# Kernel optimization log

Measured on AMD Instinct MI355X. Metric: run time of the kernel, lower is better.

The kernel has to match this reference:

```python
import jax, jax.numpy as jnp
import numpy as np

N = 100000   # nodes
E = 1600000  # edges (avg degree 16)
D = 64       # node_dim == edge_dim == graph_width == emb_dim
L = 3        # num_layer


def setup_inputs() -> dict:
    key = jax.random.key(0)
    ks = jax.random.split(key, 7)
    x = jax.random.normal(ks[0], (N, D), dtype=jnp.float32)
    edge_index = jax.random.randint(ks[1], (2, E), 0, N, dtype=jnp.int32)
    edge_attr = jax.random.normal(ks[2], (E, D), dtype=jnp.float32)
    # per-layer MLP params: Linear(2D -> 2D), ReLU, Linear(2D -> D)
    s1 = 1.0 / np.sqrt(2 * D)
    W1 = jax.random.normal(ks[3], (L, 2 * D, 2 * D), dtype=jnp.float32) * s1
    b1 = jnp.zeros((L, 2 * D), dtype=jnp.float32)
    W2 = jax.random.normal(ks[4], (L, 2 * D, D), dtype=jnp.float32) * s1
    b2 = jnp.zeros((L, D), dtype=jnp.float32)
    return {"x": x, "edge_index": edge_index, "edge_attr": edge_attr,
            "W1": W1, "b1": b1, "W2": W2, "b2": b2}


def reference(x, edge_index, edge_attr, W1, b1, W2, b2):
    n = x.shape[0]
    loop = jnp.arange(n, dtype=edge_index.dtype)
    src = jnp.concatenate([edge_index[0], loop])   # x_j = x[src]
    dst = jnp.concatenate([edge_index[1], loop])   # aggregate at dst
    # self-loop edge attr: zeros with last column = 1
    sl_attr = jnp.zeros((n, edge_attr.shape[1]), x.dtype).at[:, -1].set(1.0)
    ea = jnp.concatenate([edge_attr, sl_attr], axis=0)  # [E+N, D]

    h = x
    for l in range(L):
        msg = jnp.concatenate([ea, h[src]], axis=1)              # [E+N, 2D]
        aggr = jax.ops.segment_sum(msg, dst, num_segments=n)     # [N, 2D]
        hid = jnp.maximum(aggr @ W1[l] + b1[l], 0.0)             # [N, 2D]
        h_new = hid @ W2[l] + b2[l]                              # [N, D]
        if l < L - 1:                                            # ReLU between layers (JK='last')
            h_new = jnp.maximum(h_new, 0.0)
        h = h_new
    return h
```

## Files before the change

### kernel.cpp

```cpp
#include <hip/hip_runtime.h>

typedef unsigned int uint;
typedef unsigned short ushort;

#define WS_ALIGN(x) (((x) + (size_t)255) & ~(size_t)255)

typedef __attribute__((ext_vector_type(8))) short short8;
typedef __attribute__((ext_vector_type(4))) float f32x4;

__device__ __forceinline__ ushort f2bf(float f) {
    uint u = __builtin_bit_cast(uint, f);
    u = (u + 0x7fffu + ((u >> 16) & 1u)) >> 16;
    return (ushort)u;
}
__device__ __forceinline__ uint packbf(float a, float b) {
    return (uint)f2bf(a) | ((uint)f2bf(b) << 16);
}
__device__ __forceinline__ float bflo(uint u) { return __builtin_bit_cast(float, u << 16); }
__device__ __forceinline__ float bfhi(uint u) { return __builtin_bit_cast(float, u & 0xffff0000u); }

__global__ __launch_bounds__(256) void k_prep(const float4* __restrict__ x, ushort4* __restrict__ xh, int n4,
                                              const float* __restrict__ W1, ushort* __restrict__ W1t, int t1,
                                              const float* __restrict__ W2, ushort* __restrict__ W2t, int t2,
                                              int* __restrict__ cnt, int N) {
    int i = blockIdx.x * 256 + threadIdx.x;
    if (i < n4) {
        float4 v = x[i];
        ushort4 o;
        o.x = f2bf(v.x); o.y = f2bf(v.y); o.z = f2bf(v.z); o.w = f2bf(v.w);
        xh[i] = o;
        return;
    }
    int j = i - n4;
    if (j < t1) {
        int kk = j & 127;
        int rem = j >> 7;
        int nn = rem % 128;
        int l = rem / 128;
        W1t[j] = f2bf(W1[((size_t)(l * 128 + kk)) * 128 + nn]);
        return;
    }
    int k2 = j - t1;
    if (k2 < t2) {
        int kk = k2 & 127;
        int rem = k2 >> 7;
        int nn = rem % 64;
        int l = rem / 64;
        W2t[k2] = f2bf(W2[((size_t)(l * 128 + kk)) * 64 + nn]);
        return;
    }
    int z = k2 - t2;
    if (z < N) cnt[z] = 0;
}

__global__ __launch_bounds__(256) void k_fill(const int* __restrict__ ei, int* __restrict__ cnt,
                                              int2* __restrict__ csr, int E) {
    int i = blockIdx.x * 256 + threadIdx.x;
    int e0 = i * 2;
    if (e0 >= E) return;
    int2 ss = *(const int2*)(ei + e0);
    int2 dd = *(const int2*)(ei + E + e0);
    {
        int p = atomicAdd(&cnt[dd.x], 1);
        if (p < 64) csr[((size_t)dd.x << 6) + p] = make_int2(ss.x, e0);
    }
    if (e0 + 1 < E) {
        int p = atomicAdd(&cnt[dd.y], 1);
        if (p < 64) csr[((size_t)dd.y << 6) + p] = make_int2(ss.y, e0 + 1);
    }
}

__device__ __forceinline__ void aggr_edge_body(int wid, int lane, const float* __restrict__ ea,
                                               const int* __restrict__ cnt, const int2* __restrict__ csr,
                                               ushort* __restrict__ aggr_e) {
    const f32x4* ea4 = (const f32x4*)ea;
    const int q = lane >> 4, t = lane & 15;
    int m = cnt[wid]; m = m > 64 ? 64 : m;
    int idx = (lane < m) ? csr[((size_t)wid << 6) + lane].y : 0;
    f32x4 s = (f32x4)(0.f);
    if (q == 0 && t == 15) s[3] = 1.0f;
    int j = 0;
    for (; j + 16 <= m; j += 16) {
        int e0 = __shfl(idx, j + q),     e1 = __shfl(idx, j + 4 + q);
        int e2 = __shfl(idx, j + 8 + q), e3 = __shfl(idx, j + 12 + q);
        f32x4 v0 = __builtin_nontemporal_load(&ea4[(size_t)e0 * 16 + t]);
        f32x4 v1 = __builtin_nontemporal_load(&ea4[(size_t)e1 * 16 + t]);
        f32x4 v2 = __builtin_nontemporal_load(&ea4[(size_t)e2 * 16 + t]);
        f32x4 v3 = __builtin_nontemporal_load(&ea4[(size_t)e3 * 16 + t]);
        s += (v0 + v1) + (v2 + v3);
    }
    for (; j + 4 <= m; j += 4) {
        int e0 = __shfl(idx, j + q);
        s += __builtin_nontemporal_load(&ea4[(size_t)e0 * 16 + t]);
    }
    if (j < m) {
        int e0 = __shfl(idx, j + q);
        if (j + q < m) s += __builtin_nontemporal_load(&ea4[(size_t)e0 * 16 + t]);
    }
    s[0] += __shfl_xor(s[0], 16); s[1] += __shfl_xor(s[1], 16);
    s[2] += __shfl_xor(s[2], 16); s[3] += __shfl_xor(s[3], 16);
    s[0] += __shfl_xor(s[0], 32); s[1] += __shfl_xor(s[1], 32);
    s[2] += __shfl_xor(s[2], 32); s[3] += __shfl_xor(s[3], 32);
    if (q == 0) {
        uint2 o;
        o.x = packbf(s[0], s[1]);
        o.y = packbf(s[2], s[3]);
        *(uint2*)(aggr_e + (size_t)wid * 64 + t * 4) = o;
    }
}

__device__ __forceinline__ void aggr_h_body(int wid, int lane, const ushort* __restrict__ h,
                                            const int* __restrict__ cnt, const int2* __restrict__ csr,
                                            ushort* __restrict__ aggr_h) {
    const uint2* h2 = (const uint2*)h;
    const int q = lane >> 4, t = lane & 15;
    int m = cnt[wid]; m = m > 64 ? 64 : m;
    int idx = (lane < m) ? csr[((size_t)wid << 6) + lane].x : 0;
    float s0 = 0.f, s1 = 0.f, s2 = 0.f, s3 = 0.f;
    if (q == 0) {
        uint2 u = h2[(size_t)wid * 16 + t];
        s0 = bflo(u.x); s1 = bfhi(u.x); s2 = bflo(u.y); s3 = bfhi(u.y);
    }
    int j = 0;
    for (; j + 16 <= m; j += 16) {
        int r0 = __shfl(idx, j + q),     r1 = __shfl(idx, j + 4 + q);
        int r2 = __shfl(idx, j + 8 + q), r3 = __shfl(idx, j + 12 + q);
        uint2 u0 = h2[(size_t)r0 * 16 + t];
        uint2 u1 = h2[(size_t)r1 * 16 + t];
        uint2 u2 = h2[(size_t)r2 * 16 + t];
        uint2 u3 = h2[(size_t)r3 * 16 + t];
        s0 += (bflo(u0.x) + bflo(u1.x)) + (bflo(u2.x) + bflo(u3.x));
        s1 += (bfhi(u0.x) + bfhi(u1.x)) + (bfhi(u2.x) + bfhi(u3.x));
        s2 += (bflo(u0.y) + bflo(u1.y)) + (bflo(u2.y) + bflo(u3.y));
        s3 += (bfhi(u0.y) + bfhi(u1.y)) + (bfhi(u2.y) + bfhi(u3.y));
    }
    for (; j + 4 <= m; j += 4) {
        int r0 = __shfl(idx, j + q);
        uint2 u = h2[(size_t)r0 * 16 + t];
        s0 += bflo(u.x); s1 += bfhi(u.x); s2 += bflo(u.y); s3 += bfhi(u.y);
    }
    if (j < m) {
        int r0 = __shfl(idx, j + q);
        if (j + q < m) {
            uint2 u = h2[(size_t)r0 * 16 + t];
            s0 += bflo(u.x); s1 += bfhi(u.x); s2 += bflo(u.y); s3 += bfhi(u.y);
        }
    }
    s0 += __shfl_xor(s0, 16); s1 += __shfl_xor(s1, 16);
    s2 += __shfl_xor(s2, 16); s3 += __shfl_xor(s3, 16);
    s0 += __shfl_xor(s0, 32); s1 += __shfl_xor(s1, 32);
    s2 += __shfl_xor(s2, 32); s3 += __shfl_xor(s3, 32);
    if (q == 0) {
        uint2 o;
        o.x = packbf(s0, s1);
        o.y = packbf(s2, s3);
        *(uint2*)(aggr_h + (size_t)wid * 64 + t * 4) = o;
    }
}

__global__ __launch_bounds__(256) void k_aggr_combo(const float* __restrict__ ea, const ushort* __restrict__ xh,
                                                    const int* __restrict__ cnt, const int2* __restrict__ csr,
                                                    ushort* __restrict__ aggr_e, ushort* __restrict__ aggr_h,
                                                    int n, int gN4) {
    int lane = threadIdx.x & 63;
    if ((int)blockIdx.x < gN4) {
        int wid = (blockIdx.x * 256 + threadIdx.x) >> 6;
        if (wid < n) aggr_edge_body(wid, lane, ea, cnt, csr, aggr_e);
    } else {
        int wid = ((blockIdx.x - gN4) * 256 + threadIdx.x) >> 6;
        if (wid < n) aggr_h_body(wid, lane, xh, cnt, csr, aggr_h);
    }
}

__global__ __launch_bounds__(256) void k_aggr_h(const ushort* __restrict__ h, const int* __restrict__ cnt,
                                                const int2* __restrict__ csr, ushort* __restrict__ aggr_h, int n) {
    int wid = (blockIdx.x * 256 + threadIdx.x) >> 6;
    int lane = threadIdx.x & 63;
    if (wid >= n) return;
    aggr_h_body(wid, lane, h, cnt, csr, aggr_h);
}

__global__ __launch_bounds__(256) void k_mlp(const ushort* __restrict__ aggr_e,
                                             const ushort* __restrict__ aggr_h,
                                             const ushort* __restrict__ W1t,
                                             const float* __restrict__ b1,
                                             const ushort* __restrict__ W2t,
                                             const float* __restrict__ b2,
                                             float* __restrict__ outf,
                                             ushort* __restrict__ outh,
                                             int n) {
    __shared__ ushort a_s[64][136];
    const int tid = threadIdx.x;
    const int lane = tid & 63;
    const int wv = tid >> 6;
    const int row0 = blockIdx.x * 64;
    const int mrow0 = wv * 16;

    {
        int cc = (lane & 7) * 8;
        int rr = lane >> 3;
#pragma unroll
        for (int p = 0; p < 2; ++p) {
            int r = mrow0 + p * 8 + rr;
            int node = row0 + r;
            short8 ve = (short8)(0), vh = (short8)(0);
            if (node < n) {
                ve = *(const short8*)(aggr_e + (size_t)node * 64 + cc);
                vh = *(const short8*)(aggr_h + (size_t)node * 64 + cc);
            }
            *(short8*)(&a_s[r][cc]) = ve;
            *(short8*)(&a_s[r][64 + cc]) = vh;
        }
    }

    const int arow = mrow0 + (lane & 15);
    const int koff = (lane >> 4) * 8;
    const int drow = mrow0 + (lane >> 4) * 4;

    f32x4 acc[8];
#pragma unroll
    for (int nt = 0; nt < 8; ++nt) acc[nt] = (f32x4)(0.f);
    for (int ks = 0; ks < 4; ++ks) {
        short8 af = *(const short8*)(&a_s[arow][ks * 32 + koff]);
#pragma unroll
        for (int nt = 0; nt < 8; ++nt) {
            short8 bf = *(const short8*)(W1t + (size_t)(nt * 16 + (lane & 15)) * 128 + ks * 32 + koff);
            acc[nt] = __builtin_amdgcn_mfma_f32_16x16x32_bf16(af, bf, acc[nt], 0, 0, 0);
        }
    }
#pragma unroll
    for (int nt = 0; nt < 8; ++nt) {
        int col = nt * 16 + (lane & 15);
        float bias = b1[col];
#pragma unroll
        for (int r = 0; r < 4; ++r) {
            float v = acc[nt][r] + bias;
            v = v > 0.f ? v : 0.f;
            a_s[drow + r][col] = f2bf(v);
        }
    }

    f32x4 acc2[4];
#pragma unroll
    for (int nt = 0; nt < 4; ++nt) acc2[nt] = (f32x4)(0.f);
    for (int ks = 0; ks < 4; ++ks) {
        short8 af = *(const short8*)(&a_s[arow][ks * 32 + koff]);
#pragma unroll
        for (int nt = 0; nt < 4; ++nt) {
            short8 bf = *(const short8*)(W2t + (size_t)(nt * 16 + (lane & 15)) * 128 + ks * 32 + koff);
            acc2[nt] = __builtin_amdgcn_mfma_f32_16x16x32_bf16(af, bf, acc2[nt], 0, 0, 0);
        }
    }
#pragma unroll
    for (int nt = 0; nt < 4; ++nt) {
        int col = nt * 16 + (lane & 15);
        float bias = b2[col];
#pragma unroll
        for (int r = 0; r < 4; ++r) {
            int grow = row0 + drow + r;
            if (grow < n) {
                float v = acc2[nt][r] + bias;
                if (outh) {
                    v = v > 0.f ? v : 0.f;
                    outh[(size_t)grow * 64 + col] = f2bf(v);
                } else {
                    outf[(size_t)grow * 64 + col] = v;
                }
            }
        }
    }
}

extern "C" void kernel_launch(void* const* d_in, const int* in_sizes, int n_in,
                              void* d_out, int out_size, void* d_ws, size_t ws_size,
                              hipStream_t stream) {
    const float* x  = (const float*)d_in[0];
    const int*   ei = (const int*)d_in[1];
    const float* ea = (const float*)d_in[2];
    const float* W1 = (const float*)d_in[3];
    const float* b1 = (const float*)d_in[4];
    const float* W2 = (const float*)d_in[5];
    const float* b2 = (const float*)d_in[6];
    const int N = in_sizes[0] / 64;
    const int E = in_sizes[1] / 2;
    const int L = in_sizes[3] / (128 * 128);

    char* ws = (char*)d_ws;
    size_t o = 0;
    auto carve = [&](size_t bytes) { char* p = ws + o; o += WS_ALIGN(bytes); return p; };
    int*    cnt     = (int*)carve((size_t)N * 4);
    int2*   csr     = (int2*)carve((size_t)N * 64 * 8);
    ushort* aggr_e  = (ushort*)carve((size_t)N * 64 * 2);
    ushort* aggr_h  = (ushort*)carve((size_t)N * 64 * 2);
    ushort* xh      = (ushort*)carve((size_t)N * 64 * 2);
    ushort* hA      = (ushort*)carve((size_t)N * 64 * 2);
    ushort* hB      = (ushort*)carve((size_t)N * 64 * 2);
    ushort* W1t     = (ushort*)carve((size_t)L * 128 * 128 * 2);
    ushort* W2t     = (ushort*)carve((size_t)L * 64 * 128 * 2);

    int n4 = N * 16;
    int t1 = L * 128 * 128;
    int t2 = L * 64 * 128;
    int prep_total = n4 + t1 + t2 + N;
    k_prep<<<(prep_total + 255) / 256, 256, 0, stream>>>((const float4*)x, (ushort4*)xh, n4,
                                                         W1, W1t, t1, W2, W2t, t2, cnt, N);

    int gF = ((E + 1) / 2 + 255) / 256;
    k_fill<<<gF, 256, 0, stream>>>(ei, cnt, csr, E);

    int gN4 = (N + 3) / 4;
    k_aggr_combo<<<2 * gN4, 256, 0, stream>>>(ea, xh, cnt, csr, aggr_e, aggr_h, N, gN4);

    int gM = (N + 63) / 64;
    for (int l = 0; l < L; ++l) {
        if (l > 0) {
            const ushort* hin = (l == 1) ? hA : hB;
            k_aggr_h<<<gN4, 256, 0, stream>>>(hin, cnt, csr, aggr_h, N);
        }
        float*  outf = (l == L - 1) ? (float*)d_out : nullptr;
        ushort* outh = (l == L - 1) ? nullptr : ((l == 0) ? hA : hB);
        k_mlp<<<gM, 256, 0, stream>>>(aggr_e, aggr_h,
                                      W1t + (size_t)l * 128 * 128, b1 + (size_t)l * 128,
                                      W2t + (size_t)l * 64 * 128, b2 + (size_t)l * 64,
                                      outf, outh, N);
    }
}
```

Measured before the change: 473.4 us.

## Fuse neighbor-h aggregation into the MLP kernel for layers after the first

For layers 1 and 2, the separate k_aggr_h pass is replaced by one 1024-thread kernel. Each wave gathers and sums neighbor h rows for four nodes straight into shared memory, then runs both MFMA GEMMs on the 64-row tile, with the hidden activations also held in shared memory. This removes the aggr_h round trip through global memory and one launch per layer. In exchange, each block runs the latency-bound gather serially across only 16 waves, and the larger blocks may lower occupancy or the gather's memory-level parallelism.

```diff
diff --git a/kernel.cpp b/kernel.cpp
--- a/kernel.cpp
+++ b/kernel.cpp
@@ -109,16 +109,15 @@
     }
 }
 
-__device__ __forceinline__ void aggr_h_body(int wid, int lane, const ushort* __restrict__ h,
-                                            const int* __restrict__ cnt, const int2* __restrict__ csr,
-                                            ushort* __restrict__ aggr_h) {
+__device__ __forceinline__ uint2 aggr_h_vals(int node, int lane, const ushort* __restrict__ h,
+                                             const int* __restrict__ cnt, const int2* __restrict__ csr) {
     const uint2* h2 = (const uint2*)h;
     const int q = lane >> 4, t = lane & 15;
-    int m = cnt[wid]; m = m > 64 ? 64 : m;
-    int idx = (lane < m) ? csr[((size_t)wid << 6) + lane].x : 0;
+    int m = cnt[node]; m = m > 64 ? 64 : m;
+    int idx = (lane < m) ? csr[((size_t)node << 6) + lane].x : 0;
     float s0 = 0.f, s1 = 0.f, s2 = 0.f, s3 = 0.f;
     if (q == 0) {
-        uint2 u = h2[(size_t)wid * 16 + t];
+        uint2 u = h2[(size_t)node * 16 + t];
         s0 = bflo(u.x); s1 = bfhi(u.x); s2 = bflo(u.y); s3 = bfhi(u.y);
     }
     int j = 0;
@@ -150,12 +149,17 @@
     s2 += __shfl_xor(s2, 16); s3 += __shfl_xor(s3, 16);
     s0 += __shfl_xor(s0, 32); s1 += __shfl_xor(s1, 32);
     s2 += __shfl_xor(s2, 32); s3 += __shfl_xor(s3, 32);
-    if (q == 0) {
-        uint2 o;
-        o.x = packbf(s0, s1);
-        o.y = packbf(s2, s3);
-        *(uint2*)(aggr_h + (size_t)wid * 64 + t * 4) = o;
-    }
+    uint2 o;
+    o.x = packbf(s0, s1);
+    o.y = packbf(s2, s3);
+    return o;
+}
+
+__device__ __forceinline__ void aggr_h_body(int wid, int lane, const ushort* __restrict__ h,
+                                            const int* __restrict__ cnt, const int2* __restrict__ csr,
+                                            ushort* __restrict__ aggr_h) {
+    uint2 o = aggr_h_vals(wid, lane, h, cnt, csr);
+    if ((lane >> 4) == 0) *(uint2*)(aggr_h + (size_t)wid * 64 + (lane & 15) * 4) = o;
 }
 
 __global__ __launch_bounds__(256) void k_aggr_combo(const float* __restrict__ ea, const ushort* __restrict__ xh,
@@ -172,23 +176,10 @@
     }
 }
 
-__global__ __launch_bounds__(256) void k_aggr_h(const ushort* __restrict__ h, const int* __restrict__ cnt,
-                                                const int2* __restrict__ csr, ushort* __restrict__ aggr_h, int n) {
-    int wid = (blockIdx.x * 256 + threadIdx.x) >> 6;
-    int lane = threadIdx.x & 63;
-    if (wid >= n) return;
-    aggr_h_body(wid, lane, h, cnt, csr, aggr_h);
-}
-
-__global__ __launch_bounds__(256) void k_mlp(const ushort* __restrict__ aggr_e,
-                                             const ushort* __restrict__ aggr_h,
-                                             const ushort* __restrict__ W1t,
-                                             const float* __restrict__ b1,
-                                             const ushort* __restrict__ W2t,
-                                             const float* __restrict__ b2,
-                                             float* __restrict__ outf,
-                                             ushort* __restrict__ outh,
-                                             int n) {
+__global__ __launch_bounds__(256) void k_mlp(const ushort* __restrict__ aggr_e, const ushort* __restrict__ aggr_h,
+                                             const ushort* __restrict__ W1t, const float* __restrict__ b1,
+                                             const ushort* __restrict__ W2t, const float* __restrict__ b2,
+                                             float* __restrict__ outf, ushort* __restrict__ outh, int n) {
     __shared__ ushort a_s[64][136];
     const int tid = threadIdx.x;
     const int lane = tid & 63;
@@ -260,6 +251,93 @@
             int grow = row0 + drow + r;
             if (grow < n) {
                 float v = acc2[nt][r] + bias;
+                if (outh) {
+                    v = v > 0.f ? v : 0.f;
+                    outh[(size_t)grow * 64 + col] = f2bf(v);
+                } else {
+                    outf[(size_t)grow * 64 + col] = v;
+                }
+            }
+        }
+    }
+}
+
+__global__ __launch_bounds__(1024) void k_layer_fused(const ushort* __restrict__ h,
+                                                      const ushort* __restrict__ aggr_e,
+                                                      const int* __restrict__ cnt, const int2* __restrict__ csr,
+                                                      const ushort* __restrict__ W1t, const float* __restrict__ b1,
+                                                      const ushort* __restrict__ W2t, const float* __restrict__ b2,
+                                                      float* __restrict__ outf, ushort* __restrict__ outh, int n) {
+    __shared__ ushort a_s[64][136];
+    __shared__ ushort hid_s[64][136];
+    const int tid = threadIdx.x;
+    const int lane = tid & 63;
+    const int wv = tid >> 6;
+    const int row0 = blockIdx.x * 64;
+
+    {
+        int r = tid >> 4;
+        int c4 = (tid & 15) * 4;
+        int node = row0 + r;
+        ushort4 v = make_ushort4(0, 0, 0, 0);
+        if (node < n) v = *(const ushort4*)(aggr_e + (size_t)node * 64 + c4);
+        *(ushort4*)(&a_s[r][c4]) = v;
+    }
+
+    {
+        const int t = lane & 15;
+        for (int i = 0; i < 4; ++i) {
+            int r = wv * 4 + i;
+            int node = row0 + r;
+            uint2 o = make_uint2(0u, 0u);
+            if (node < n) o = aggr_h_vals(node, lane, h, cnt, csr);
+            if ((lane >> 4) == 0) *(uint2*)(&a_s[r][64 + t * 4]) = o;
+        }
+    }
+    __syncthreads();
+
+    const int rg = wv >> 2, cg = wv & 3;
+    const int arow = rg * 16 + (lane & 15);
+    const int koff = (lane >> 4) * 8;
+    const int drow = rg * 16 + (lane >> 4) * 4;
+
+    f32x4 acc[2];
+    acc[0] = (f32x4)(0.f); acc[1] = (f32x4)(0.f);
+    for (int ks = 0; ks < 4; ++ks) {
+        short8 af = *(const short8*)(&a_s[arow][ks * 32 + koff]);
+#pragma unroll
+        for (int nt = 0; nt < 2; ++nt) {
+            short8 bf = *(const short8*)(W1t + (size_t)(cg * 32 + nt * 16 + (lane & 15)) * 128 + ks * 32 + koff);
+            acc[nt] = __builtin_amdgcn_mfma_f32_16x16x32_bf16(af, bf, acc[nt], 0, 0, 0);
+        }
+    }
+#pragma unroll
+    for (int nt = 0; nt < 2; ++nt) {
+        int col = cg * 32 + nt * 16 + (lane & 15);
+        float bias = b1[col];
+#pragma unroll
+        for (int r = 0; r < 4; ++r) {
+            float v = acc[nt][r] + bias;
+            v = v > 0.f ? v : 0.f;
+            hid_s[drow + r][col] = f2bf(v);
+        }
+    }
+    __syncthreads();
+
+    f32x4 acc2 = (f32x4)(0.f);
+    for (int ks = 0; ks < 4; ++ks) {
+        short8 af = *(const short8*)(&hid_s[arow][ks * 32 + koff]);
+        short8 bf = *(const short8*)(W2t + (size_t)(cg * 16 + (lane & 15)) * 128 + ks * 32 + koff);
+        acc2 = __builtin_amdgcn_mfma_f32_16x16x32_bf16(af, bf, acc2, 0, 0, 0);
+    }
+    {
+        int col = cg * 16 + (lane & 15);
+        float bias = b2[col];
+#pragma unroll
+        for (int r = 0; r < 4; ++r) {
+            int grow = row0 + drow + r;
+            if (grow < n) {
+                float v = acc2[r] + bias;
                 if (outh) {
                     v = v > 0.f ? v : 0.f;
                     outh[(size_t)grow * 64 + col] = f2bf(v);
@@ -313,15 +391,17 @@
 
     int gM = (N + 63) / 64;
     for (int l = 0; l < L; ++l) {
-        if (l > 0) {
-            const ushort* hin = (l == 1) ? hA : hB;
-            k_aggr_h<<<gN4, 256, 0, stream>>>(hin, cnt, csr, aggr_h, N);
-        }
         float*  outf = (l == L - 1) ? (float*)d_out : nullptr;
-        ushort* outh = (l == L - 1) ? nullptr : ((l == 0) ? hA : hB);
-        k_mlp<<<gM, 256, 0, stream>>>(aggr_e, aggr_h,
-                                      W1t + (size_t)l * 128 * 128, b1 + (size_t)l * 128,
-                                      W2t + (size_t)l * 64 * 128, b2 + (size_t)l * 64,
-                                      outf, outh, N);
-    }
-}
+        ushort* outh = (l == L - 1) ? nullptr : ((l & 1) ? hB : hA);
+        if (l == 0) {
+            k_mlp<<<gM, 256, 0, stream>>>(aggr_e, aggr_h,
+                                          W1t, b1, W2t, b2, outf, outh, N);
+        } else {
+            const ushort* hin = (l & 1) ? hA : hB;
+            k_layer_fused<<<gM, 1024, 0, stream>>>(hin, aggr_e, cnt, csr,
+                                                   W1t + (size_t)l * 128 * 128, b1 + (size_t)l * 128,
+                                                   W2t + (size_t)l * 64 * 128, b2 + (size_t)l * 64,
+                                                   outf, outh, N);
+        }
+    }
+}
```

New measurement: 473.1 us. About the same (-0.1%).
